# Kernel optimization log

Hardware: AMD Instinct MI355X
Metric: run time of the kernel (lower is better)

Reference implementation:

```python
import jax, jax.numpy as jnp
import numpy as np

NUM_NODES = 100000
EMBED_DIM = 64
NUM_LAYERS = 3
NUM_EDGES = 3200000


def setup_inputs() -> dict:
    key = jax.random.key(0)
    k1, k2 = jax.random.split(key)
    # xavier_uniform for [N, D]: bound = sqrt(6/(N+D))
    bound = float(np.sqrt(6.0 / (NUM_NODES + EMBED_DIM)))
    emb = jax.random.uniform(k1, (NUM_NODES, EMBED_DIM), dtype=jnp.float32,
                             minval=-bound, maxval=bound)
    edge_index = jax.random.randint(k2, (2, NUM_EDGES), 0, NUM_NODES, dtype=jnp.int64)
    return {"emb": emb, "edge_index": edge_index}


def reference(emb, edge_index):
    # LightGCN: xs = [x0, LGConv(x0), LGConv^2(x0), ...]; output = mean(xs)
    # LGConv (PyG, add_self_loops=False): out[i] = sum_{(j,i) in E} x[j] / sqrt(d_j * d_i)
    n = emb.shape[0]
    row, col = edge_index[0], edge_index[1]  # row = source j, col = target i
    ones = jnp.ones(row.shape[0], dtype=emb.dtype)
    deg = jax.ops.segment_sum(ones, col, num_segments=n)  # in-degree per gcn_norm
    dinv = jnp.where(deg > 0, jax.lax.rsqrt(jnp.where(deg > 0, deg, 1.0)), 0.0)
    norm = dinv[row] * dinv[col]  # [E]

    x = emb
    acc = emb
    for _ in range(NUM_LAYERS):
        msgs = x[row] * norm[:, None]                      # gather + normalize [E, D]
        x = jax.ops.segment_sum(msgs, col, num_segments=n)  # scatter-add [N, D]
        acc = acc + x
    return acc / (NUM_LAYERS + 1)
```

## Files before the change

### kernel.cpp

```cpp
#include <hip/hip_runtime.h>
#include <hip/hip_bf16.h>
#include <hip/hip_fp16.h>
#include <stdint.h>


#define N_NODES 100000
#define N_EDGES 3200000
#define DIM 64

#define NB 196
#define BSH 9
#define BNODES 512
#define CAP 20480

#define CHUNK 4096
#define NBLK1 ((N_EDGES + CHUNK - 1) / CHUNK)

__global__ __launch_bounds__(256) void k_bucket(const int* __restrict__ ei,
                                                int* __restrict__ gcursor,
                                                int* __restrict__ staging) {
    __shared__ int stage[CHUNK];
    __shared__ unsigned char sbkt[CHUNK];
    __shared__ int bcnt[NB];
    __shared__ int boff[NB];
    __shared__ int bstart[NB];
    __shared__ int gbase[NB];
    __shared__ int wt[4];

    int t = threadIdx.x;
    int e0 = blockIdx.x * CHUNK;
    int nblk = min(CHUNK, N_EDGES - e0);
    int nvec = nblk >> 2;

    const int4* col4 = (const int4*)(ei + N_EDGES + e0);
    const int4* row4 = (const int4*)(ei + e0);

    for (int i = t; i < NB; i += 256) { bcnt[i] = 0; boff[i] = 0; }
    __syncthreads();

    for (int i = t; i < nvec; i += 256) {
        int4 c = col4[i];
        atomicAdd(&bcnt[c.x >> BSH], 1);
        atomicAdd(&bcnt[c.y >> BSH], 1);
        atomicAdd(&bcnt[c.z >> BSH], 1);
        atomicAdd(&bcnt[c.w >> BSH], 1);
    }
    __syncthreads();

    {
        int v = (t < NB) ? bcnt[t] : 0;
        int lane = t & 63, w = t >> 6;
        int s = v;
#pragma unroll
        for (int off = 1; off < 64; off <<= 1) {
            int u = __shfl_up(s, off);
            if (lane >= off) s += u;
        }
        if (lane == 63) wt[w] = s;
        __syncthreads();
        int wo = 0;
        for (int ww = 0; ww < w; ww++) wo += wt[ww];
        if (t < NB) {
            bstart[t] = s - v + wo;
            gbase[t] = (v > 0) ? atomicAdd(&gcursor[t], v) : 0;
        }
    }
    __syncthreads();

    for (int i = t; i < nvec; i += 256) {
        int4 c = col4[i];
        int4 r = row4[i];
        int b0 = c.x >> BSH, b1 = c.y >> BSH, b2 = c.z >> BSH, b3 = c.w >> BSH;
        int p0 = bstart[b0] + atomicAdd(&boff[b0], 1);
        int p1 = bstart[b1] + atomicAdd(&boff[b1], 1);
        int p2 = bstart[b2] + atomicAdd(&boff[b2], 1);
        int p3 = bstart[b3] + atomicAdd(&boff[b3], 1);
        stage[p0] = (r.x << BSH) | (c.x & (BNODES - 1)); sbkt[p0] = (unsigned char)b0;
        stage[p1] = (r.y << BSH) | (c.y & (BNODES - 1)); sbkt[p1] = (unsigned char)b1;
        stage[p2] = (r.z << BSH) | (c.z & (BNODES - 1)); sbkt[p2] = (unsigned char)b2;
        stage[p3] = (r.w << BSH) | (c.w & (BNODES - 1)); sbkt[p3] = (unsigned char)b3;
    }
    __syncthreads();

    for (int i = t; i < nblk; i += 256) {
        int e = stage[i];
        int b = sbkt[i];
        staging[(size_t)b * CAP + gbase[b] + (i - bstart[b])] = e;
    }
}

__global__ void k_bstart(const int* __restrict__ gcursor, int* __restrict__ bucketStart) {
    __shared__ int wt[4];
    int t = threadIdx.x;
    int v = (t < NB) ? gcursor[t] : 0;
    int lane = t & 63, w = t >> 6;
    int s = v;
#pragma unroll
    for (int off = 1; off < 64; off <<= 1) {
        int u = __shfl_up(s, off);
        if (lane >= off) s += u;
    }
    if (lane == 63) wt[w] = s;
    __syncthreads();
    int wo = 0;
    for (int ww = 0; ww < w; ww++) wo += wt[ww];
    if (t < NB) bucketStart[t] = s - v + wo;
}

__global__ __launch_bounds__(256) void k_build(const int* __restrict__ gcursor,
                                               const int* __restrict__ bucketStart,
                                               const int* __restrict__ staging,
                                               int* __restrict__ deg,
                                               int* __restrict__ base,
                                               float* __restrict__ dinv,
                                               int* __restrict__ csrc) {
    __shared__ int ldeg[BNODES];
    __shared__ int lcur[BNODES];
    __shared__ int wt[4];

    int b = blockIdx.x;
    int t = threadIdx.x;
    int n0 = b << BSH;
    int nloc = min(BNODES, N_NODES - n0);
    int cnt = gcursor[b];
    const int* st = staging + (size_t)b * CAP;

    ldeg[t] = 0; ldeg[t + 256] = 0;
    __syncthreads();

    for (int i = t; i < cnt; i += 256) {
        atomicAdd(&ldeg[st[i] & (BNODES - 1)], 1);
    }
    __syncthreads();

    int a0 = ldeg[2 * t], a1 = ldeg[2 * t + 1];
    int s = a0 + a1;
    int lane = t & 63, w = t >> 6;
    int ss = s;
#pragma unroll
    for (int off = 1; off < 64; off <<= 1) {
        int u = __shfl_up(ss, off);
        if (lane >= off) ss += u;
    }
    if (lane == 63) wt[w] = ss;
    __syncthreads();
    int wo = 0;
    for (int ww = 0; ww < w; ww++) wo += wt[ww];
    int excl = ss - s + wo;

    int gb = bucketStart[b] + excl;
    int n = n0 + 2 * t;
    lcur[2 * t] = gb;
    lcur[2 * t + 1] = gb + a0;
    if (2 * t < nloc) {
        deg[n] = a0;
        base[n] = gb;
        dinv[n] = (a0 > 0) ? rsqrtf((float)a0) : 0.0f;
    }
    if (2 * t + 1 < nloc) {
        deg[n + 1] = a1;
        base[n + 1] = gb + a0;
        dinv[n + 1] = (a1 > 0) ? rsqrtf((float)a1) : 0.0f;
    }
    __syncthreads();

    for (int i = t; i < cnt; i += 256) {
        int e = st[i];
        int p = atomicAdd(&lcur[e & (BNODES - 1)], 1);
        csrc[p] = e >> BSH;
    }
}

__global__ void k_z0(const float* __restrict__ emb, const float* __restrict__ dinv,
                     __half* __restrict__ zA, __half* __restrict__ zB) {
    const int total = (N_NODES * DIM) / 4;
    int i = blockIdx.x * blockDim.x + threadIdx.x;
    if (i >= total) {
        int r = i - total;
        if (r < 16) ((uint2*)(zA + (size_t)N_NODES * DIM))[r] = make_uint2(0, 0);
        else if (r < 32) ((uint2*)(zB + (size_t)N_NODES * DIM))[r - 16] = make_uint2(0, 0);
        return;
    }
    float di = dinv[(i * 4) >> 6];
    const float4 v = ((const float4*)emb)[i];
    union { ushort h[4]; uint2 u; } pk;
    __half h0 = __float2half(v.x * di);
    __half h1 = __float2half(v.y * di);
    __half h2 = __float2half(v.z * di);
    __half h3 = __float2half(v.w * di);
    pk.h[0] = *(ushort*)&h0; pk.h[1] = *(ushort*)&h1;
    pk.h[2] = *(ushort*)&h2; pk.h[3] = *(ushort*)&h3;
    ((uint2*)zA)[i] = pk.u;
}

__global__ __launch_bounds__(256) void k_spmv(
    const int* __restrict__ base, const int* __restrict__ deg,
    const int* __restrict__ csrc, const __half* __restrict__ z,
    const float* __restrict__ dinv, __half* __restrict__ znext,
    const float* __restrict__ emb, float* __restrict__ acc_out, int mode) {
    int wave = (blockIdx.x * blockDim.x + threadIdx.x) >> 6;
    int lane = threadIdx.x & 63;
    if (wave >= N_NODES) return;
    int g = lane >> 3;
    int l = lane & 7;

    int start = base[wave];
    int cnt = deg[wave];
    float di = dinv[wave];
    int ng = (cnt + 7) >> 3;

    __half2 hz = __float2half2_rn(0.0f);
    __half2 hacc0 = hz, hacc1 = hz, hacc2 = hz, hacc3 = hz;

#define GLOAD(KK, SVAR)                              \
    int e##SVAR = (KK) * 8 + g;                      \
    int SVAR = csrc[start + e##SVAR];                \
    SVAR = (e##SVAR < cnt) ? SVAR : N_NODES;

#define GACC(SVAR)                                                        \
    do {                                                                  \
        uint4 v = *((const uint4*)(z + ((size_t)SVAR << 6)) + l);         \
        const __half2* hv = (const __half2*)&v;                           \
        hacc0 = __hadd2(hacc0, hv[0]);                                    \
        hacc1 = __hadd2(hacc1, hv[1]);                                    \
        hacc2 = __hadd2(hacc2, hv[2]);                                    \
        hacc3 = __hadd2(hacc3, hv[3]);                                    \
    } while (0)

    int k = 0;
    for (; k + 4 <= ng; k += 4) {
        GLOAD(k + 0, s0); GLOAD(k + 1, s1); GLOAD(k + 2, s2); GLOAD(k + 3, s3);
        GACC(s0); GACC(s1); GACC(s2); GACC(s3);
    }
    int rem = ng - k;
    if (rem > 0) {
        GLOAD(k + 0, t0);
        if (rem > 1) { GLOAD(k + 1, t1);
            if (rem > 2) { GLOAD(k + 2, t2); GACC(t0); GACC(t1); GACC(t2); }
            else { GACC(t0); GACC(t1); }
        } else { GACC(t0); }
    }
#undef GLOAD
#undef GACC

#pragma unroll
    for (int off = 8; off <= 32; off <<= 1) {
        int b0 = __shfl_xor(*(int*)&hacc0, off);
        int b1 = __shfl_xor(*(int*)&hacc1, off);
        int b2 = __shfl_xor(*(int*)&hacc2, off);
        int b3 = __shfl_xor(*(int*)&hacc3, off);
        hacc0 = __hadd2(hacc0, *(__half2*)&b0);
        hacc1 = __hadd2(hacc1, *(__half2*)&b1);
        hacc2 = __hadd2(hacc2, *(__half2*)&b2);
        hacc3 = __hadd2(hacc3, *(__half2*)&b3);
    }

    if (lane < 8) {
        size_t o = (size_t)wave * DIM + lane * 8;
        float xo[8];
        xo[0] = __low2float(hacc0) * di; xo[1] = __high2float(hacc0) * di;
        xo[2] = __low2float(hacc1) * di; xo[3] = __high2float(hacc1) * di;
        xo[4] = __low2float(hacc2) * di; xo[5] = __high2float(hacc2) * di;
        xo[6] = __low2float(hacc3) * di; xo[7] = __high2float(hacc3) * di;

        float4 o0, o1;
        if (mode == 0) {
            float4 e0 = ((const float4*)(emb + o))[0];
            float4 e1 = ((const float4*)(emb + o))[1];
            o0 = make_float4(e0.x + xo[0], e0.y + xo[1], e0.z + xo[2], e0.w + xo[3]);
            o1 = make_float4(e1.x + xo[4], e1.y + xo[5], e1.z + xo[6], e1.w + xo[7]);
        } else if (mode == 1) {
            float4 a0 = ((const float4*)(acc_out + o))[0];
            float4 a1 = ((const float4*)(acc_out + o))[1];
            o0 = make_float4(a0.x + xo[0], a0.y + xo[1], a0.z + xo[2], a0.w + xo[3]);
            o1 = make_float4(a1.x + xo[4], a1.y + xo[5], a1.z + xo[6], a1.w + xo[7]);
        } else {
            float4 a0 = ((const float4*)(acc_out + o))[0];
            float4 a1 = ((const float4*)(acc_out + o))[1];
            o0 = make_float4((a0.x + xo[0]) * 0.25f, (a0.y + xo[1]) * 0.25f,
                             (a0.z + xo[2]) * 0.25f, (a0.w + xo[3]) * 0.25f);
            o1 = make_float4((a1.x + xo[4]) * 0.25f, (a1.y + xo[5]) * 0.25f,
                             (a1.z + xo[6]) * 0.25f, (a1.w + xo[7]) * 0.25f);
        }
        ((float4*)(acc_out + o))[0] = o0;
        ((float4*)(acc_out + o))[1] = o1;

        if (mode != 2) {
            union { ushort h[8]; uint4 u; } pk;
#pragma unroll
            for (int j = 0; j < 8; j++) {
                __half hh = __float2half(xo[j] * di);
                pk.h[j] = *(ushort*)&hh;
            }
            *((uint4*)(znext + o)) = pk.u;
        }
    }
}

extern "C" void kernel_launch(void* const* d_in, const int* in_sizes, int n_in,
                              void* d_out, int out_size, void* d_ws, size_t ws_size,
                              hipStream_t stream) {
    const float* emb = (const float*)d_in[0];
    const int* ei = (const int*)d_in[1];
    float* out = (float*)d_out;

    char* ws = (char*)d_ws;
    size_t off = 0;
    auto alloc = [&](size_t bytes) -> void* {
        void* p = ws + off;
        off += (bytes + 511) & ~(size_t)511;
        return p;
    };
    int* deg = (int*)alloc((size_t)N_NODES * 4);
    float* dinv = (float*)alloc((size_t)N_NODES * 4);
    int* base = (int*)alloc((size_t)N_NODES * 4);
    int* gcursor = (int*)alloc(NB * 4);
    int* bucketStart = (int*)alloc(NB * 4);
    int* csrc = (int*)alloc(((size_t)N_EDGES + 64) * 4);
    size_t zbytes = (size_t)(N_NODES + 1) * DIM * 2;
    size_t stbytes = (size_t)NB * CAP * 4;
    char* transient = (char*)alloc(stbytes > zbytes ? stbytes : zbytes);
    int* staging = (int*)transient;
    __half* zA = (__half*)transient;
    __half* zB = (__half*)alloc(zbytes);

    hipMemsetAsync(gcursor, 0, NB * 4, stream);

    k_bucket<<<NBLK1, 256, 0, stream>>>(ei, gcursor, staging);
    k_bstart<<<1, 256, 0, stream>>>(gcursor, bucketStart);
    k_build<<<NB, 256, 0, stream>>>(gcursor, bucketStart, staging, deg, base, dinv, csrc);
    k_z0<<<(N_NODES * DIM / 4) / 256 + 1, 256, 0, stream>>>(emb, dinv, zA, zB);

    int spmvBlocks = (N_NODES + 3) / 4;
    k_spmv<<<spmvBlocks, 256, 0, stream>>>(base, deg, csrc, zA, dinv, zB, emb, out, 0);
    k_spmv<<<spmvBlocks, 256, 0, stream>>>(base, deg, csrc, zB, dinv, zA, emb, out, 1);
    k_spmv<<<spmvBlocks, 256, 0, stream>>>(base, deg, csrc, zA, dinv, zB, emb, out, 2);
}
```

Baseline: 324.7 us.

## Drop per-layer accumulator traffic, pack node records, and use smaller build buckets

The first two SpMV layers no longer read and write the fp32 output accumulator. They only produce the next half-precision scaled embedding. The final layer rebuilds layers 1 and 2 from the two stored half-precision z buffers, multiplied by sqrt(deg), and combines them with emb and x3. Per-node start, degree and dinv are packed into a single int4 record so each wave does one load instead of three. Build buckets shrink from 512 to 128 nodes (782 buckets), and the scans now handle four buckets per thread. The cost is extra fp16 rounding in the reconstructed intermediate layers, plus a tighter per-bucket staging capacity.

```diff
diff --git a/kernel.cpp b/kernel.cpp
--- a/kernel.cpp
+++ b/kernel.cpp
@@ -8,10 +8,10 @@
 #define N_EDGES 3200000
 #define DIM 64
 
-#define NB 196
-#define BSH 9
-#define BNODES 512
-#define CAP 20480
+#define BSH 7
+#define BNODES 128
+#define NB 782
+#define CAP 4608
 
 #define CHUNK 4096
 #define NBLK1 ((N_EDGES + CHUNK - 1) / CHUNK)
@@ -20,12 +20,12 @@
                                                 int* __restrict__ gcursor,
                                                 int* __restrict__ staging) {
     __shared__ int stage[CHUNK];
-    __shared__ unsigned char sbkt[CHUNK];
+    __shared__ unsigned short sbkt[CHUNK];
     __shared__ int bcnt[NB];
     __shared__ int boff[NB];
     __shared__ int bstart[NB];
     __shared__ int gbase[NB];
-    __shared__ int wt[4];
+    __shared__ int wtt[4];
 
     int t = threadIdx.x;
     int e0 = blockIdx.x * CHUNK;
@@ -48,21 +48,34 @@
     __syncthreads();
 
     {
-        int v = (t < NB) ? bcnt[t] : 0;
+        int v[4];
+        int s = 0;
+#pragma unroll
+        for (int k = 0; k < 4; k++) {
+            int j = t * 4 + k;
+            v[k] = (j < NB) ? bcnt[j] : 0;
+            s += v[k];
+        }
         int lane = t & 63, w = t >> 6;
-        int s = v;
+        int ss = s;
 #pragma unroll
         for (int off = 1; off < 64; off <<= 1) {
-            int u = __shfl_up(s, off);
-            if (lane >= off) s += u;
-        }
-        if (lane == 63) wt[w] = s;
+            int u = __shfl_up(ss, off);
+            if (lane >= off) ss += u;
+        }
+        if (lane == 63) wtt[w] = ss;
         __syncthreads();
         int wo = 0;
-        for (int ww = 0; ww < w; ww++) wo += wt[ww];
-        if (t < NB) {
-            bstart[t] = s - v + wo;
-            gbase[t] = (v > 0) ? atomicAdd(&gcursor[t], v) : 0;
+        for (int ww = 0; ww < w; ww++) wo += wtt[ww];
+        int run = ss - s + wo;
+#pragma unroll
+        for (int k = 0; k < 4; k++) {
+            int j = t * 4 + k;
+            if (j < NB) {
+                bstart[j] = run;
+                gbase[j] = (v[k] > 0) ? atomicAdd(&gcursor[j], v[k]) : 0;
+            }
+            run += v[k];
         }
     }
     __syncthreads();
@@ -75,10 +88,10 @@
         int p1 = bstart[b1] + atomicAdd(&boff[b1], 1);
         int p2 = bstart[b2] + atomicAdd(&boff[b2], 1);
         int p3 = bstart[b3] + atomicAdd(&boff[b3], 1);
-        stage[p0] = (r.x << BSH) | (c.x & (BNODES - 1)); sbkt[p0] = (unsigned char)b0;
-        stage[p1] = (r.y << BSH) | (c.y & (BNODES - 1)); sbkt[p1] = (unsigned char)b1;
-        stage[p2] = (r.z << BSH) | (c.z & (BNODES - 1)); sbkt[p2] = (unsigned char)b2;
-        stage[p3] = (r.w << BSH) | (c.w & (BNODES - 1)); sbkt[p3] = (unsigned char)b3;
+        stage[p0] = (r.x << BSH) | (c.x & (BNODES - 1)); sbkt[p0] = (unsigned short)b0;
+        stage[p1] = (r.y << BSH) | (c.y & (BNODES - 1)); sbkt[p1] = (unsigned short)b1;
+        stage[p2] = (r.z << BSH) | (c.z & (BNODES - 1)); sbkt[p2] = (unsigned short)b2;
+        stage[p3] = (r.w << BSH) | (c.w & (BNODES - 1)); sbkt[p3] = (unsigned short)b3;
     }
     __syncthreads();
 
@@ -90,33 +103,45 @@
 }
 
 __global__ void k_bstart(const int* __restrict__ gcursor, int* __restrict__ bucketStart) {
-    __shared__ int wt[4];
+    __shared__ int wtt[4];
     int t = threadIdx.x;
-    int v = (t < NB) ? gcursor[t] : 0;
+    int v[4];
+    int s = 0;
+#pragma unroll
+    for (int k = 0; k < 4; k++) {
+        int j = t * 4 + k;
+        v[k] = (j < NB) ? gcursor[j] : 0;
+        s += v[k];
+    }
     int lane = t & 63, w = t >> 6;
-    int s = v;
+    int ss = s;
 #pragma unroll
     for (int off = 1; off < 64; off <<= 1) {
-        int u = __shfl_up(s, off);
-        if (lane >= off) s += u;
-    }
-    if (lane == 63) wt[w] = s;
+        int u = __shfl_up(ss, off);
+        if (lane >= off) ss += u;
+    }
+    if (lane == 63) wtt[w] = ss;
     __syncthreads();
     int wo = 0;
-    for (int ww = 0; ww < w; ww++) wo += wt[ww];
-    if (t < NB) bucketStart[t] = s - v + wo;
+    for (int ww = 0; ww < w; ww++) wo += wtt[ww];
+    int run = ss - s + wo;
+#pragma unroll
+    for (int k = 0; k < 4; k++) {
+        int j = t * 4 + k;
+        if (j < NB) bucketStart[j] = run;
+        run += v[k];
+    }
 }
 
 __global__ __launch_bounds__(256) void k_build(const int* __restrict__ gcursor,
                                                const int* __restrict__ bucketStart,
                                                const int* __restrict__ staging,
-                                               int* __restrict__ deg,
-                                               int* __restrict__ base,
+                                               int4* __restrict__ rec,
                                                float* __restrict__ dinv,
                                                int* __restrict__ csrc) {
     __shared__ int ldeg[BNODES];
     __shared__ int lcur[BNODES];
-    __shared__ int wt[4];
+    __shared__ int wtt[4];
 
     int b = blockIdx.x;
     int t = threadIdx.x;
@@ -125,7 +150,7 @@
     int cnt = gcursor[b];
     const int* st = staging + (size_t)b * CAP;
 
-    ldeg[t] = 0; ldeg[t + 256] = 0;
+    if (t < BNODES) ldeg[t] = 0;
     __syncthreads();
 
     for (int i = t; i < cnt; i += 256) {
@@ -133,34 +158,29 @@
     }
     __syncthreads();
 
-    int a0 = ldeg[2 * t], a1 = ldeg[2 * t + 1];
-    int s = a0 + a1;
+    int a = (t < BNODES) ? ldeg[t] : 0;
     int lane = t & 63, w = t >> 6;
-    int ss = s;
+    int ss = a;
 #pragma unroll
     for (int off = 1; off < 64; off <<= 1) {
         int u = __shfl_up(ss, off);
         if (lane >= off) ss += u;
     }
-    if (lane == 63) wt[w] = ss;
+    if (lane == 63) wtt[w] = ss;
     __syncthreads();
     int wo = 0;
-    for (int ww = 0; ww < w; ww++) wo += wt[ww];
-    int excl = ss - s + wo;
-
+    for (int ww = 0; ww < w; ww++) wo += wtt[ww];
+    int excl = ss - a + wo;
     int gb = bucketStart[b] + excl;
-    int n = n0 + 2 * t;
-    lcur[2 * t] = gb;
-    lcur[2 * t + 1] = gb + a0;
-    if (2 * t < nloc) {
-        deg[n] = a0;
-        base[n] = gb;
-        dinv[n] = (a0 > 0) ? rsqrtf((float)a0) : 0.0f;
-    }
-    if (2 * t + 1 < nloc) {
-        deg[n + 1] = a1;
-        base[n + 1] = gb + a0;
-        dinv[n + 1] = (a1 > 0) ? rsqrtf((float)a1) : 0.0f;
+
+    if (t < BNODES) {
+        lcur[t] = gb;
+        if (t < nloc) {
+            int n = n0 + t;
+            float di = (a > 0) ? rsqrtf((float)a) : 0.0f;
+            rec[n] = make_int4(gb, a, __float_as_int(di), 0);
+            dinv[n] = di;
+        }
     }
     __syncthreads();
 
@@ -194,19 +214,20 @@
 }
 
 __global__ __launch_bounds__(256) void k_spmv(
-    const int* __restrict__ base, const int* __restrict__ deg,
-    const int* __restrict__ csrc, const __half* __restrict__ z,
-    const float* __restrict__ dinv, __half* __restrict__ znext,
-    const float* __restrict__ emb, float* __restrict__ acc_out, int mode) {
+    const int4* __restrict__ rec, const int* __restrict__ csrc,
+    const __half* __restrict__ z, __half* __restrict__ znext,
+    const __half* __restrict__ zprev, const float* __restrict__ emb,
+    float* __restrict__ out, int mode) {
     int wave = (blockIdx.x * blockDim.x + threadIdx.x) >> 6;
     int lane = threadIdx.x & 63;
     if (wave >= N_NODES) return;
     int g = lane >> 3;
     int l = lane & 7;
 
-    int start = base[wave];
-    int cnt = deg[wave];
-    float di = dinv[wave];
+    int4 nr = rec[wave];
+    int start = nr.x;
+    int cnt = nr.y;
+    float di = __int_as_float(nr.z);
     int ng = (cnt + 7) >> 3;
 
     __half2 hz = __float2half2_rn(0.0f);
@@ -257,42 +278,48 @@
 
     if (lane < 8) {
         size_t o = (size_t)wave * DIM + lane * 8;
-        float xo[8];
-        xo[0] = __low2float(hacc0) * di; xo[1] = __high2float(hacc0) * di;
-        xo[2] = __low2float(hacc1) * di; xo[3] = __high2float(hacc1) * di;
-        xo[4] = __low2float(hacc2) * di; xo[5] = __high2float(hacc2) * di;
-        xo[6] = __low2float(hacc3) * di; xo[7] = __high2float(hacc3) * di;
-
-        float4 o0, o1;
+        float x[8];
+        x[0] = __low2float(hacc0) * di; x[1] = __high2float(hacc0) * di;
+        x[2] = __low2float(hacc1) * di; x[3] = __high2float(hacc1) * di;
+        x[4] = __low2float(hacc2) * di; x[5] = __high2float(hacc2) * di;
+        x[6] = __low2float(hacc3) * di; x[7] = __high2float(hacc3) * di;
+
         if (mode == 0) {
-            float4 e0 = ((const float4*)(emb + o))[0];
-            float4 e1 = ((const float4*)(emb + o))[1];
-            o0 = make_float4(e0.x + xo[0], e0.y + xo[1], e0.z + xo[2], e0.w + xo[3]);
-            o1 = make_float4(e1.x + xo[4], e1.y + xo[5], e1.z + xo[6], e1.w + xo[7]);
-        } else if (mode == 1) {
-            float4 a0 = ((const float4*)(acc_out + o))[0];
-            float4 a1 = ((const float4*)(acc_out + o))[1];
-            o0 = make_float4(a0.x + xo[0], a0.y + xo[1], a0.z + xo[2], a0.w + xo[3]);
-            o1 = make_float4(a1.x + xo[4], a1.y + xo[5], a1.z + xo[6], a1.w + xo[7]);
-        } else {
-            float4 a0 = ((const float4*)(acc_out + o))[0];
-            float4 a1 = ((const float4*)(acc_out + o))[1];
-            o0 = make_float4((a0.x + xo[0]) * 0.25f, (a0.y + xo[1]) * 0.25f,
-                             (a0.z + xo[2]) * 0.25f, (a0.w + xo[3]) * 0.25f);
-            o1 = make_float4((a1.x + xo[4]) * 0.25f, (a1.y + xo[5]) * 0.25f,
-                             (a1.z + xo[6]) * 0.25f, (a1.w + xo[7]) * 0.25f);
-        }
-        ((float4*)(acc_out + o))[0] = o0;
-        ((float4*)(acc_out + o))[1] = o1;
-
-        if (mode != 2) {
             union { ushort h[8]; uint4 u; } pk;
 #pragma unroll
             for (int j = 0; j < 8; j++) {
-                __half hh = __float2half(xo[j] * di);
+                __half hh = __float2half(x[j] * di);
                 pk.h[j] = *(ushort*)&hh;
             }
             *((uint4*)(znext + o)) = pk.u;
+        } else {
+            float sdeg = (cnt > 0) ? sqrtf((float)cnt) : 0.0f;
+            uint4 v2 = *((const uint4*)(zprev + o));
+            uint4 v3 = *((const uint4*)(z + o));
+            const __half2* h2 = (const __half2*)&v2;
+            const __half2* h3 = (const __half2*)&v3;
+            float4 e0 = ((const float4*)(emb + o))[0];
+            float4 e1 = ((const float4*)(emb + o))[1];
+            float zs[8];
+#pragma unroll
+            for (int j = 0; j < 4; j++) {
+                float2 a2 = __half22float2(h2[j]);
+                float2 a3 = __half22float2(h3[j]);
+                zs[2 * j] = a2.x + a3.x;
+                zs[2 * j + 1] = a2.y + a3.y;
+            }
+            float4 o0 = make_float4(
+                (e0.x + sdeg * zs[0] + x[0]) * 0.25f,
+                (e0.y + sdeg * zs[1] + x[1]) * 0.25f,
+                (e0.z + sdeg * zs[2] + x[2]) * 0.25f,
+                (e0.w + sdeg * zs[3] + x[3]) * 0.25f);
+            float4 o1 = make_float4(
+                (e1.x + sdeg * zs[4] + x[4]) * 0.25f,
+                (e1.y + sdeg * zs[5] + x[5]) * 0.25f,
+                (e1.z + sdeg * zs[6] + x[6]) * 0.25f,
+                (e1.w + sdeg * zs[7] + x[7]) * 0.25f);
+            ((float4*)(out + o))[0] = o0;
+            ((float4*)(out + o))[1] = o1;
         }
     }
 }
@@ -311,9 +338,8 @@
         off += (bytes + 511) & ~(size_t)511;
         return p;
     };
-    int* deg = (int*)alloc((size_t)N_NODES * 4);
+    int4* rec = (int4*)alloc((size_t)N_NODES * 16);
     float* dinv = (float*)alloc((size_t)N_NODES * 4);
-    int* base = (int*)alloc((size_t)N_NODES * 4);
     int* gcursor = (int*)alloc(NB * 4);
     int* bucketStart = (int*)alloc(NB * 4);
     int* csrc = (int*)alloc(((size_t)N_EDGES + 64) * 4);
@@ -328,11 +354,11 @@
 
     k_bucket<<<NBLK1, 256, 0, stream>>>(ei, gcursor, staging);
     k_bstart<<<1, 256, 0, stream>>>(gcursor, bucketStart);
-    k_build<<<NB, 256, 0, stream>>>(gcursor, bucketStart, staging, deg, base, dinv, csrc);
+    k_build<<<NB, 256, 0, stream>>>(gcursor, bucketStart, staging, rec, dinv, csrc);
     k_z0<<<(N_NODES * DIM / 4) / 256 + 1, 256, 0, stream>>>(emb, dinv, zA, zB);
 
     int spmvBlocks = (N_NODES + 3) / 4;
-    k_spmv<<<spmvBlocks, 256, 0, stream>>>(base, deg, csrc, zA, dinv, zB, emb, out, 0);
-    k_spmv<<<spmvBlocks, 256, 0, stream>>>(base, deg, csrc, zB, dinv, zA, emb, out, 1);
-    k_spmv<<<spmvBlocks, 256, 0, stream>>>(base, deg, csrc, zA, dinv, zB, emb, out, 2);
-}
+    k_spmv<<<spmvBlocks, 256, 0, stream>>>(rec, csrc, zA, zB, nullptr, emb, out, 0);
+    k_spmv<<<spmvBlocks, 256, 0, stream>>>(rec, csrc, zB, zA, nullptr, emb, out, 0);
+    k_spmv<<<spmvBlocks, 256, 0, stream>>>(rec, csrc, zA, nullptr, zB, emb, out, 2);
+}
```

Result: slower. 337.0 us (+3.8%).
